# Kernel optimization log

Hardware: AMD Instinct MI355X
Metric: run time of the kernel (lower is better)

## Reference

```python
import jax, jax.numpy as jnp
import numpy as np

D_K = 64
EPS = 1e-6


def setup_inputs() -> dict:
    key = jax.random.key(0)
    ks = jax.random.split(key, 6)
    B, S, D2, DV = 4, 2048, 1024, 64
    q = jax.random.normal(ks[0], (B, S, D2), dtype=jnp.float32)
    k = jax.random.normal(ks[1], (B, S, D2), dtype=jnp.float32)
    v = jax.random.normal(ks[2], (B, S, D2), dtype=jnp.float32)
    mask = jax.random.randint(ks[3], (B, S, S), 0, 2) == 1
    V = jax.random.normal(ks[4], (1, DV), dtype=jnp.float32)
    fc_w = jax.random.normal(ks[5], (D2, DV), dtype=jnp.float32) * (1.0 / np.sqrt(DV))
    fc_b = jnp.zeros((D2,), dtype=jnp.float32)
    ln_g = jnp.ones((D2,), dtype=jnp.float32)
    ln_b = jnp.zeros((D2,), dtype=jnp.float32)
    return {"q": q, "k": k, "v": v, "mask": mask, "V": V,
            "fc_w": fc_w, "fc_b": fc_b, "ln_g": ln_g, "ln_b": ln_b}


def _layer_norm(x, g, b):
    mu = jnp.mean(x, axis=-1, keepdims=True)
    var = jnp.var(x, axis=-1, keepdims=True)
    return (x - mu) * jax.lax.rsqrt(var + EPS) * g + b


def reference(q, k, v, mask, V, fc_w, fc_b, ln_g, ln_b):
    residual = q
    qn = _layer_norm(q, ln_g, ln_b)
    # scaled dot-product scores (no softmax in this variant)
    attn = jnp.einsum('bsd,btd->bst', qn / jnp.sqrt(jnp.float32(D_K)), k)
    attn = jnp.where(mask, 0.0, attn)  # masked_fill with 0
    # v_ = V broadcast over (batch, seq, key); attn @ v_ == row-sum outer V
    output = jnp.sum(attn, axis=-1, keepdims=True) * V  # [B,S,d_v]
    output = output @ fc_w.T + fc_b                     # [B,S,2*d_model]
    output = output + residual
    return (output, attn)
```

## Files before the change

kernel.cpp:

```cpp
#include <hip/hip_runtime.h>
#include <hip/hip_bf16.h>
#include <cstdint>

#define S_LEN 2048
#define D2_   1024
#define DV_   64
#define NB_   4

typedef __bf16 bf16x8 __attribute__((ext_vector_type(8)));
typedef float  f32x4  __attribute__((ext_vector_type(4)));

__device__ __forceinline__ unsigned short f2bf(float f) {
  union { float f; unsigned int u; } v; v.f = f;
  unsigned int r = v.u + 0x7fffu + ((v.u >> 16) & 1u);
  return (unsigned short)(r >> 16);
}

__device__ __forceinline__ void async16(const unsigned short* g, unsigned short* l) {
  __builtin_amdgcn_global_load_lds(
      (__attribute__((address_space(1))) void*)g,
      (__attribute__((address_space(3))) void*)l,
      16, 0, 0);
}

__global__ void __launch_bounds__(256) prep_kernel(
    const float* __restrict__ q, const float* __restrict__ k,
    const float* __restrict__ gam, const float* __restrict__ bet,
    const float* __restrict__ V, const float* __restrict__ fw,
    unsigned short* __restrict__ qn, unsigned short* __restrict__ kb,
    float* __restrict__ w2, float* __restrict__ rowsum) {
  const int row = blockIdx.x;
  const int t = threadIdx.x;

  if (row < 32) rowsum[row * 256 + t] = 0.0f;

  const float4 x = ((const float4*)(q + (size_t)row * D2_))[t];
  float s  = x.x + x.y + x.z + x.w;
  float ss = x.x * x.x + x.y * x.y + x.z * x.z + x.w * x.w;
  #pragma unroll
  for (int o = 32; o > 0; o >>= 1) { s += __shfl_down(s, o); ss += __shfl_down(ss, o); }
  __shared__ float red[8];
  if ((t & 63) == 0) { red[t >> 6] = s; red[(t >> 6) + 4] = ss; }
  __syncthreads();
  const float tot  = red[0] + red[1] + red[2] + red[3];
  const float tots = red[4] + red[5] + red[6] + red[7];
  const float mu  = tot * (1.0f / D2_);
  const float var = tots * (1.0f / D2_) - mu * mu;
  const float rs  = rsqrtf(var + 1e-6f) * 0.125f;
  const float4 gv = ((const float4*)gam)[t];
  const float4 bv = ((const float4*)bet)[t];
  ushort4 o4;
  o4.x = f2bf((x.x - mu) * rs * gv.x + 0.125f * bv.x);
  o4.y = f2bf((x.y - mu) * rs * gv.y + 0.125f * bv.y);
  o4.z = f2bf((x.z - mu) * rs * gv.z + 0.125f * bv.z);
  o4.w = f2bf((x.w - mu) * rs * gv.w + 0.125f * bv.w);
  ((ushort4*)(qn + (size_t)row * D2_))[t] = o4;

  const float4 kx = ((const float4*)(k + (size_t)row * D2_))[t];
  ushort4 k4;
  k4.x = f2bf(kx.x); k4.y = f2bf(kx.y); k4.z = f2bf(kx.z); k4.w = f2bf(kx.w);
  ((ushort4*)(kb + (size_t)row * D2_))[t] = k4;

  if (row < 4) {
    const int d = row * 256 + t;
    const float4* r  = (const float4*)(fw + (size_t)d * DV_);
    const float4* vv = (const float4*)V;
    float acc = 0.f;
    #pragma unroll
    for (int j = 0; j < 16; ++j) {
      const float4 a = r[j], b = vv[j];
      acc += a.x * b.x + a.y * b.y + a.z * b.z + a.w * b.w;
    }
    w2[d] = acc;
  }
}

__global__ void __launch_bounds__(512, 4) attn_gemm_kernel(
    const unsigned short* __restrict__ qn,
    const unsigned short* __restrict__ kb,
    const int* __restrict__ mask,
    float* __restrict__ attn,
    float* __restrict__ rowsum) {
  __shared__ __align__(16) unsigned short Asm_[2 * 8192];
  __shared__ __align__(16) unsigned short Bsm_[2 * 8192];

  const int t  = threadIdx.x;
  const int bn = blockIdx.x * 128;
  const int bm = blockIdx.y * 128;
  const int bt = blockIdx.z;

  const int srow_ = t >> 3;
  const int pg_   = (t & 7) ^ (srow_ & 7);
  const unsigned short* gA = qn + ((size_t)bt * S_LEN + bm + srow_) * D2_ + pg_ * 8;
  const unsigned short* gB = kb + ((size_t)bt * S_LEN + bn + srow_) * D2_ + pg_ * 8;
  unsigned short* lA = Asm_ + t * 8;
  unsigned short* lB = Bsm_ + t * 8;

  const int lane = t & 63;
  const int w  = t >> 6;
  const int wm = (w >> 2) * 64;
  const int wn = (w & 3) * 32;
  const int lr = lane & 15;
  const int lg = lane >> 4;

  const int m_base = bm + wm + lr;
  const size_t rb0 = ((size_t)bt * S_LEN) * S_LEN;
  int4 mk[4][2];
  #pragma unroll
  for (int fm = 0; fm < 4; ++fm)
    #pragma unroll
    for (int fn = 0; fn < 2; ++fn)
      mk[fm][fn] = *(const int4*)(mask + rb0 + (size_t)(m_base + fm * 16) * S_LEN
                                  + bn + wn + fn * 16 + lg * 4);

  f32x4 acc[4][2] = {};

  for (int k0 = 0; k0 < D2_; k0 += 128) {
    #pragma unroll
    for (int j = 0; j < 4; ++j) {
      const int h = j >> 1, rh = j & 1;
      const size_t gofs = (size_t)rh * 64 * D2_ + h * 64;
      const int    lofs = h * 8192 + rh * 4096;
      async16(gA + gofs, lA + lofs);
      async16(gB + gofs, lB + lofs);
    }
    gA += 128; gB += 128;
    __syncthreads();

    #pragma unroll
    for (int ks = 0; ks < 4; ++ks) {
      const int pl = (ks >> 1) * 8192;
      const int sl = (((ks & 1) << 2) + lg) ^ (lr & 7);
      bf16x8 af[4], bfv[2];
      #pragma unroll
      for (int f = 0; f < 4; ++f)
        af[f]  = *(const bf16x8*)(Asm_ + pl + (wm + f * 16 + lr) * 64 + sl * 8);
      #pragma unroll
      for (int f = 0; f < 2; ++f)
        bfv[f] = *(const bf16x8*)(Bsm_ + pl + (wn + f * 16 + lr) * 64 + sl * 8);
      #pragma unroll
      for (int fm = 0; fm < 4; ++fm)
        #pragma unroll
        for (int fn = 0; fn < 2; ++fn)
          acc[fm][fn] = __builtin_amdgcn_mfma_f32_16x16x32_bf16(
              bfv[fn], af[fm], acc[fm][fn], 0, 0, 0);
    }
    __syncthreads();
  }

  #pragma unroll
  for (int fm = 0; fm < 4; ++fm) {
    const int m = m_base + fm * 16;
    const size_t rowbase = rb0 + (size_t)m * S_LEN;
    float s = 0.f;
    #pragma unroll
    for (int fn = 0; fn < 2; ++fn) {
      const int n0 = bn + wn + fn * 16 + lg * 4;
      float4 v;
      v.x = mk[fm][fn].x ? 0.0f : acc[fm][fn][0];
      v.y = mk[fm][fn].y ? 0.0f : acc[fm][fn][1];
      v.z = mk[fm][fn].z ? 0.0f : acc[fm][fn][2];
      v.w = mk[fm][fn].w ? 0.0f : acc[fm][fn][3];
      *(float4*)(attn + rowbase + n0) = v;
      s += v.x + v.y + v.z + v.w;
    }
    s += __shfl_xor(s, 16);
    s += __shfl_xor(s, 32);
    if (lane < 16) atomicAdd(rowsum + (size_t)bt * S_LEN + m, s);
  }
}

__global__ void __launch_bounds__(256) out_kernel(
    const float* __restrict__ rowsum, const float* __restrict__ q,
    const float* __restrict__ w2, const float* __restrict__ fcb,
    float* __restrict__ out) {
  const int row = blockIdx.x;
  const int t = threadIdx.x;
  const float rs = rowsum[row];
  const float4 wv = ((const float4*)w2)[t];
  const float4 bv = ((const float4*)fcb)[t];
  const float4 qv = ((const float4*)(q + (size_t)row * D2_))[t];
  float4 o4;
  o4.x = rs * wv.x + bv.x + qv.x;
  o4.y = rs * wv.y + bv.y + qv.y;
  o4.z = rs * wv.z + bv.z + qv.z;
  o4.w = rs * wv.w + bv.w + qv.w;
  ((float4*)(out + (size_t)row * D2_))[t] = o4;
}

extern "C" void kernel_launch(void* const* d_in, const int* in_sizes, int n_in,
                              void* d_out, int out_size, void* d_ws, size_t ws_size,
                              hipStream_t stream) {
  (void)in_sizes; (void)n_in; (void)out_size; (void)ws_size;
  const float* q    = (const float*)d_in[0];
  const float* k    = (const float*)d_in[1];
  const int*   mask = (const int*)d_in[3];
  const float* V    = (const float*)d_in[4];
  const float* fw   = (const float*)d_in[5];
  const float* fcb  = (const float*)d_in[6];
  const float* lg   = (const float*)d_in[7];
  const float* lb   = (const float*)d_in[8];

  float* out  = (float*)d_out;
  float* attn = out + (size_t)NB_ * S_LEN * D2_;

  unsigned short* qn = (unsigned short*)out;
  unsigned short* kb = qn + (size_t)NB_ * S_LEN * D2_;
  float* w2     = (float*)d_ws;
  float* rowsum = w2 + D2_;

  prep_kernel<<<NB_ * S_LEN, 256, 0, stream>>>(q, k, lg, lb, V, fw, qn, kb, w2, rowsum);
  attn_gemm_kernel<<<dim3(S_LEN / 128, S_LEN / 128, NB_), 512, 0, stream>>>(qn, kb, mask, attn, rowsum);
  out_kernel<<<NB_ * S_LEN, 256, 0, stream>>>(rowsum, q, w2, fcb, out);
}
```

Measured before the change: 267.5 us.

## Double-buffer K-loop staging, swizzle block order, use nontemporal attn stores

Reworks the attention GEMM main loop into a two-stage pipeline over 64-wide K chunks, so async global-to-LDS loads for the next chunk are issued before computing on the current one. The first stage is issued before the mask loads to hide startup latency. Blocks are remapped so that consecutive launched blocks are spread across batches and tiles, meant to change cache/channel locality. The attn output is written with nontemporal stores to avoid polluting cache. Correctness of the single-barrier double buffering depends on the async-load ordering, since the next stage is written while other waves may still read the previous buffer.

New measurement: 271.0 us. Within noise of the previous version (+1.3%).

```diff
diff --git a/kernel.cpp b/kernel.cpp
--- a/kernel.cpp
+++ b/kernel.cpp
@@ -84,10 +84,13 @@
   __shared__ __align__(16) unsigned short Asm_[2 * 8192];
   __shared__ __align__(16) unsigned short Bsm_[2 * 8192];
 
-  const int t  = threadIdx.x;
-  const int bn = blockIdx.x * 128;
-  const int bm = blockIdx.y * 128;
-  const int bt = blockIdx.z;
+  const int t = threadIdx.x;
+
+  const int orig = blockIdx.x + 16 * (blockIdx.y + 16 * blockIdx.z);
+  const int swz  = (orig & 7) * 128 + (orig >> 3);
+  const int bn = (swz & 15) * 128;
+  const int bm = ((swz >> 4) & 15) * 128;
+  const int bt = swz >> 8;
 
   const int srow_ = t >> 3;
   const int pg_   = (t & 7) ^ (srow_ & 7);
@@ -103,6 +106,15 @@
   const int lr = lane & 15;
   const int lg = lane >> 4;
 
+  #define STAGE64(buf, koff) do {                                   \
+      async16(gA + (koff),            lA + (buf));                  \
+      async16(gA + (koff) + 64 * D2_, lA + (buf) + 4096);           \
+      async16(gB + (koff),            lB + (buf));                  \
+      async16(gB + (koff) + 64 * D2_, lB + (buf) + 4096);           \
+    } while (0)
+
+  STAGE64(0, 0);
+
   const int m_base = bm + wm + lr;
   const size_t rb0 = ((size_t)bt * S_LEN) * S_LEN;
   int4 mk[4][2];
@@ -115,22 +127,10 @@
 
   f32x4 acc[4][2] = {};
 
-  for (int k0 = 0; k0 < D2_; k0 += 128) {
-    #pragma unroll
-    for (int j = 0; j < 4; ++j) {
-      const int h = j >> 1, rh = j & 1;
-      const size_t gofs = (size_t)rh * 64 * D2_ + h * 64;
-      const int    lofs = h * 8192 + rh * 4096;
-      async16(gA + gofs, lA + lofs);
-      async16(gB + gofs, lB + lofs);
-    }
-    gA += 128; gB += 128;
-    __syncthreads();
-
-    #pragma unroll
-    for (int ks = 0; ks < 4; ++ks) {
-      const int pl = (ks >> 1) * 8192;
-      const int sl = (((ks & 1) << 2) + lg) ^ (lr & 7);
+  auto compute = [&](int pl) {
+    #pragma unroll
+    for (int ks = 0; ks < 2; ++ks) {
+      const int sl = ((ks << 2) + lg) ^ (lr & 7);
       bf16x8 af[4], bfv[2];
       #pragma unroll
       for (int f = 0; f < 4; ++f)
@@ -145,8 +145,23 @@
           acc[fm][fn] = __builtin_amdgcn_mfma_f32_16x16x32_bf16(
               bfv[fn], af[fm], acc[fm][fn], 0, 0, 0);
     }
+  };
+
+  __syncthreads();
+
+  #pragma unroll 1
+  for (int kt = 0; kt < 14; kt += 2) {
+    STAGE64(8192, (kt + 1) * 64);
+    compute(0);
+    __syncthreads();
+    STAGE64(0, (kt + 2) * 64);
+    compute(8192);
     __syncthreads();
   }
+  STAGE64(8192, 15 * 64);
+  compute(0);
+  __syncthreads();
+  compute(8192);
 
   #pragma unroll
   for (int fm = 0; fm < 4; ++fm) {
@@ -156,18 +171,19 @@
     #pragma unroll
     for (int fn = 0; fn < 2; ++fn) {
       const int n0 = bn + wn + fn * 16 + lg * 4;
-      float4 v;
-      v.x = mk[fm][fn].x ? 0.0f : acc[fm][fn][0];
-      v.y = mk[fm][fn].y ? 0.0f : acc[fm][fn][1];
-      v.z = mk[fm][fn].z ? 0.0f : acc[fm][fn][2];
-      v.w = mk[fm][fn].w ? 0.0f : acc[fm][fn][3];
-      *(float4*)(attn + rowbase + n0) = v;
-      s += v.x + v.y + v.z + v.w;
+      f32x4 v;
+      v[0] = mk[fm][fn].x ? 0.0f : acc[fm][fn][0];
+      v[1] = mk[fm][fn].y ? 0.0f : acc[fm][fn][1];
+      v[2] = mk[fm][fn].z ? 0.0f : acc[fm][fn][2];
+      v[3] = mk[fm][fn].w ? 0.0f : acc[fm][fn][3];
+      __builtin_nontemporal_store(v, (f32x4*)(attn + rowbase + n0));
+      s += v[0] + v[1] + v[2] + v[3];
     }
     s += __shfl_xor(s, 16);
     s += __shfl_xor(s, 32);
     if (lane < 16) atomicAdd(rowsum + (size_t)bt * S_LEN + m, s);
   }
+  #undef STAGE64
 }
 
 __global__ void __launch_bounds__(256) out_kernel(
```
